# Performance work log

Hardware: AMD Instinct MI355X
Metric: run time of the kernel (lower is better)

The kernel has to match this reference:

```python
import jax, jax.numpy as jnp
import numpy as np

NUM_HEADS = 8


def setup_inputs() -> dict:
    key = jax.random.key(0)
    k1, k2, k3 = jax.random.split(key, 3)
    B, C, H, W = 2, 256, 64, 64
    x = jax.random.normal(k1, (B, C, H, W), dtype=jnp.float32)
    # 1x1 conv kernels flattened to [out_ch, in_ch]
    w_qkv = jax.random.normal(k2, (3 * C, C), dtype=jnp.float32) * (1.0 / np.sqrt(C))
    w_proj = jax.random.normal(k3, (C, C), dtype=jnp.float32) * (1.0 / np.sqrt(C))
    return {"x": x, "w_qkv": w_qkv, "w_proj": w_proj}


def reference(x, w_qkv, w_proj):
    B, C, H, W = x.shape
    h = NUM_HEADS
    hc = C // h  # head_channels
    scale = hc ** (-0.5)

    # 1x1 conv == per-pixel matmul over channels
    qkv = jnp.einsum('bchw,oc->bohw', x, w_qkv)  # [B, 3C, H, W]
    q, k, v = jnp.split(qkv, 3, axis=1)          # each [B, C, H, W]

    def to_heads(t):
        # 'b (h c) x y -> b h (x y) c'
        return t.reshape(B, h, hc, H * W).transpose(0, 1, 3, 2)

    q, k, v = to_heads(q), to_heads(k), to_heads(v)  # [B, h, N, hc]

    attn = jax.nn.softmax(jnp.einsum('bhnc,bhmc->bhnm', q, k) * scale, axis=-1)
    out = jnp.einsum('bhnm,bhmc->bhnc', attn, v)     # [B, h, N, hc]

    # 'b h (x y) c -> b (h c) x y'
    out = out.transpose(0, 1, 3, 2).reshape(B, C, H, W)
    return jnp.einsum('bchw,oc->bohw', out, w_proj)
```

## Files before the change

kernel.cpp:

```cpp
#include <hip/hip_runtime.h>
#include <hip/hip_bf16.h>


typedef short s8v __attribute__((ext_vector_type(8)));
typedef float f32x16 __attribute__((ext_vector_type(16)));
typedef float f32x2 __attribute__((ext_vector_type(2)));
typedef unsigned int u32;
typedef unsigned int u32x4 __attribute__((ext_vector_type(4)));

__device__ __forceinline__ u32 cvt_pk_bf16(float lo, float hi){
  u32 d;
  asm("v_cvt_pk_bf16_f32 %0, %1, %2" : "=v"(d) : "v"(lo), "v"(hi));
  return d;
}

__device__ __forceinline__ int frag_off(int row, int c){
  return ((c>>4)<<9) + (((c>>3)&1)<<8) + (row<<3) + (c&7);
}

__global__ __launch_bounds__(256) void k_transpose_cast(const float* __restrict__ x,
                                                        __hip_bfloat16* __restrict__ xt){
  __shared__ float tile[64][65];
  const int b = blockIdx.z;
  const int c0 = blockIdx.y * 64, p0 = blockIdx.x * 64;
  const int tx = threadIdx.x & 63, ty = threadIdx.x >> 6;
  const float* src = x + ((size_t)b*256 + c0)*4096 + p0;
#pragma unroll
  for(int i=0;i<16;i++){
    int r = i*4 + ty;
    tile[r][tx] = src[(size_t)r*4096 + tx];
  }
  __syncthreads();
  __hip_bfloat16* dstb = xt + (size_t)b*1048576;
#pragma unroll
  for(int it=0; it<2; ++it){
    int id = it*256 + threadIdx.x;
    int pl = id & 63, cc = id >> 6;
    int c = c0 + cc*8;
    u32x4 wv;
    wv.x = cvt_pk_bf16(tile[cc*8+0][pl], tile[cc*8+1][pl]);
    wv.y = cvt_pk_bf16(tile[cc*8+2][pl], tile[cc*8+3][pl]);
    wv.z = cvt_pk_bf16(tile[cc*8+4][pl], tile[cc*8+5][pl]);
    wv.w = cvt_pk_bf16(tile[cc*8+6][pl], tile[cc*8+7][pl]);
    int panel = (p0 + pl) >> 5;
    *(u32x4*)(dstb + (size_t)panel*8192 + frag_off(pl & 31, c)) = wv;
  }
}

__global__ __launch_bounds__(256) void k_cast_w(const float* __restrict__ wqkv,
                                                const float* __restrict__ wproj,
                                                __hip_bfloat16* __restrict__ wq,
                                                __hip_bfloat16* __restrict__ wp){
  int e = blockIdx.x*256 + threadIdx.x;
  const float* srcw; __hip_bfloat16* dstw;
  if(e < 24576){ srcw = wqkv; dstw = wq; }
  else { e -= 24576; srcw = wproj; dstw = wp; }
  int o = e >> 5, c0 = (e & 31)*8;
  const float* s = srcw + (size_t)o*256 + c0;
  u32x4 wv;
  wv.x = cvt_pk_bf16(s[0], s[1]);
  wv.y = cvt_pk_bf16(s[2], s[3]);
  wv.z = cvt_pk_bf16(s[4], s[5]);
  wv.w = cvt_pk_bf16(s[6], s[7]);
  *(u32x4*)(dstw + (size_t)(o>>5)*8192 + frag_off(o & 31, c0)) = wv;
}

__global__ __launch_bounds__(256) void k_qkv(const __hip_bfloat16* __restrict__ w,
                                             const __hip_bfloat16* __restrict__ xt,
                                             __hip_bfloat16* __restrict__ qb,
                                             __hip_bfloat16* __restrict__ kb,
                                             __hip_bfloat16* __restrict__ vt){
  const int wave = threadIdx.x >> 6, lane = threadIdx.x & 63;
  const int l31 = lane & 31, hi = lane >> 5;
  const int t = blockIdx.x*4 + wave;
  const int ntp = t & 127, mtp = t >> 7;
  const __hip_bfloat16* a0 = w  + (size_t)(2*mtp)*8192 + lane*8;
  const __hip_bfloat16* b0 = xt + (size_t)(2*ntp)*8192 + lane*8;
  f32x16 acc00, acc01, acc10, acc11;
#pragma unroll
  for(int i=0;i<16;i++){ acc00[i]=0.f; acc01[i]=0.f; acc10[i]=0.f; acc11[i]=0.f; }
#pragma unroll
  for(int kk=0;kk<16;kk++){
    s8v af0 = *(const s8v*)(a0 + kk*512);
    s8v af1 = *(const s8v*)(a0 + 8192 + kk*512);
    s8v bf0 = *(const s8v*)(b0 + kk*512);
    s8v bf1 = *(const s8v*)(b0 + 8192 + kk*512);
    acc00 = __builtin_amdgcn_mfma_f32_32x32x16_bf16(af0, bf0, acc00, 0,0,0);
    acc01 = __builtin_amdgcn_mfma_f32_32x32x16_bf16(af0, bf1, acc01, 0,0,0);
    acc10 = __builtin_amdgcn_mfma_f32_32x32x16_bf16(af1, bf0, acc10, 0,0,0);
    acc11 = __builtin_amdgcn_mfma_f32_32x32x16_bf16(af1, bf1, acc11, 0,0,0);
  }
  const int region = mtp >> 2;
  const float s = (region==0) ? (0.17677669529663687f * 1.4426950408889634f) : 1.0f;
#pragma unroll
  for(int mi=0; mi<2; ++mi){
#pragma unroll
    for(int ni=0; ni<2; ++ni){
      const f32x16& acc = (mi==0) ? (ni==0?acc00:acc01) : (ni==0?acc10:acc11);
      const int mt = 2*mtp + mi, nt = 2*ntp + ni;
      const int bb = nt >> 7, ktile = nt & 127, h = mt & 7;
      const size_t tbase = (size_t)(bb*8 + h)*131072 + (size_t)ktile*1024;
      if(region < 2){
        __hip_bfloat16* dst = (region==0 ? qb : kb) + tbase + l31*8 + 4*hi;
#pragma unroll
        for(int g=0; g<4; ++g){
          uint2 wv;
          wv.x = cvt_pk_bf16(acc[4*g+0]*s, acc[4*g+1]*s);
          wv.y = cvt_pk_bf16(acc[4*g+2]*s, acc[4*g+3]*s);
          *(uint2*)(dst + (g>>1)*512 + (g&1)*256) = wv;
        }
      } else {
        const int j = l31 >> 4, hv = (l31 >> 2) & 1, tt = ((l31>>3)&1)*4 + (l31&3);
        __hip_bfloat16* dst = vt + tbase + j*512 + hv*256 + tt;
#pragma unroll
        for(int r=0;r<16;++r){
          int c = (r&3) + 8*(r>>2) + 4*hi;
          dst[c*8] = __float2bfloat16(acc[r]);
        }
      }
    }
  }
}

__global__ __launch_bounds__(256, 4) void k_attn(const __hip_bfloat16* __restrict__ qb,
                                                 const __hip_bfloat16* __restrict__ kb,
                                                 const __hip_bfloat16* __restrict__ vt,
                                                 __hip_bfloat16* __restrict__ ost){
  __shared__ float part[4][64][33];
  __shared__ float lsl[4][64];
  const int wave = threadIdx.x >> 6, lane = threadIdx.x & 63;
  const int l31 = lane & 31, hi = lane >> 5;
  const int vid = (blockIdx.x & 7)*128 + (blockIdx.x >> 3);
  const int bh = vid >> 6, qc = vid & 63;

  const __hip_bfloat16* qt = qb + (size_t)bh*131072 + (size_t)(qc*2)*1024 + (size_t)lane*8;
  const s8v qfA0 = *(const s8v*)qt;
  const s8v qfA1 = *(const s8v*)(qt + 512);
  const s8v qfB0 = *(const s8v*)(qt + 1024);
  const s8v qfB1 = *(const s8v*)(qt + 1536);

  const __hip_bfloat16* kbase = kb + (size_t)bh*131072 + (size_t)lane*8;
  const __hip_bfloat16* vbase = vt + (size_t)bh*131072 + (size_t)lane*8;

  f32x16 zf;
#pragma unroll
  for(int i=0;i<16;i++) zf[i]=0.f;
  f32x16 oaccA, oaccB;
#pragma unroll
  for(int i=0;i<16;i++){ oaccA[i]=0.f; oaccB[i]=0.f; }
  f32x2 sA0={0.f,0.f}, sA1={0.f,0.f}, sB0={0.f,0.f}, sB1={0.f,0.f};

  const int kt0 = wave*32;
#pragma unroll 2
  for(int i=0;i<32;++i){
    const int kt = kt0 + i;
    const __hip_bfloat16* kp = kbase + (size_t)kt*1024;
    s8v kf0 = *(const s8v*)kp, kf1 = *(const s8v*)(kp + 512);
    f32x16 saA = __builtin_amdgcn_mfma_f32_32x32x16_bf16(kf0, qfA0, zf, 0,0,0);
    saA = __builtin_amdgcn_mfma_f32_32x32x16_bf16(kf1, qfA1, saA, 0,0,0);
    f32x16 saB = __builtin_amdgcn_mfma_f32_32x32x16_bf16(kf0, qfB0, zf, 0,0,0);
    saB = __builtin_amdgcn_mfma_f32_32x32x16_bf16(kf1, qfB1, saB, 0,0,0);

    float pvA[16], pvB[16];
#pragma unroll
    for(int r=0;r<16;++r) pvA[r] = __builtin_amdgcn_exp2f(saA[r]);
#pragma unroll
    for(int r=0;r<16;++r) pvB[r] = __builtin_amdgcn_exp2f(saB[r]);
    sA0 += (f32x2){pvA[0],pvA[1]};   sA1 += (f32x2){pvA[2],pvA[3]};
    sA0 += (f32x2){pvA[4],pvA[5]};   sA1 += (f32x2){pvA[6],pvA[7]};
    sA0 += (f32x2){pvA[8],pvA[9]};   sA1 += (f32x2){pvA[10],pvA[11]};
    sA0 += (f32x2){pvA[12],pvA[13]}; sA1 += (f32x2){pvA[14],pvA[15]};
    sB0 += (f32x2){pvB[0],pvB[1]};   sB1 += (f32x2){pvB[2],pvB[3]};
    sB0 += (f32x2){pvB[4],pvB[5]};   sB1 += (f32x2){pvB[6],pvB[7]};
    sB0 += (f32x2){pvB[8],pvB[9]};   sB1 += (f32x2){pvB[10],pvB[11]};
    sB0 += (f32x2){pvB[12],pvB[13]}; sB1 += (f32x2){pvB[14],pvB[15]};

    u32x4 wA0, wA1, wB0, wB1;
    wA0.x = cvt_pk_bf16(pvA[0],  pvA[1]);   wA0.y = cvt_pk_bf16(pvA[2],  pvA[3]);
    wA0.z = cvt_pk_bf16(pvA[4],  pvA[5]);   wA0.w = cvt_pk_bf16(pvA[6],  pvA[7]);
    wA1.x = cvt_pk_bf16(pvA[8],  pvA[9]);   wA1.y = cvt_pk_bf16(pvA[10], pvA[11]);
    wA1.z = cvt_pk_bf16(pvA[12], pvA[13]);  wA1.w = cvt_pk_bf16(pvA[14], pvA[15]);
    wB0.x = cvt_pk_bf16(pvB[0],  pvB[1]);   wB0.y = cvt_pk_bf16(pvB[2],  pvB[3]);
    wB0.z = cvt_pk_bf16(pvB[4],  pvB[5]);   wB0.w = cvt_pk_bf16(pvB[6],  pvB[7]);
    wB1.x = cvt_pk_bf16(pvB[8],  pvB[9]);   wB1.y = cvt_pk_bf16(pvB[10], pvB[11]);
    wB1.z = cvt_pk_bf16(pvB[12], pvB[13]);  wB1.w = cvt_pk_bf16(pvB[14], pvB[15]);

    const __hip_bfloat16* vp = vbase + (size_t)kt*1024;
    s8v vf0 = *(const s8v*)vp, vf1 = *(const s8v*)(vp + 512);
    oaccA = __builtin_amdgcn_mfma_f32_32x32x16_bf16(vf0, __builtin_bit_cast(s8v, wA0), oaccA, 0,0,0);
    oaccA = __builtin_amdgcn_mfma_f32_32x32x16_bf16(vf1, __builtin_bit_cast(s8v, wA1), oaccA, 0,0,0);
    oaccB = __builtin_amdgcn_mfma_f32_32x32x16_bf16(vf0, __builtin_bit_cast(s8v, wB0), oaccB, 0,0,0);
    oaccB = __builtin_amdgcn_mfma_f32_32x32x16_bf16(vf1, __builtin_bit_cast(s8v, wB1), oaccB, 0,0,0);
  }

  float lsumA = (sA0.x + sA0.y) + (sA1.x + sA1.y);
  float lsumB = (sB0.x + sB0.y) + (sB1.x + sB1.y);
  lsumA += __shfl_xor(lsumA, 32, 64);
  lsumB += __shfl_xor(lsumB, 32, 64);
  lsl[wave][l31] = lsumA;
  lsl[wave][32 + l31] = lsumB;
#pragma unroll
  for(int r=0;r<16;++r){
    int c = (r&3) + 8*(r>>2) + 4*hi;
    part[wave][l31][c] = oaccA[r];
    part[wave][32 + l31][c] = oaccB[r];
  }
  __syncthreads();

  const int b = bh >> 3, h = bh & 7;
  __hip_bfloat16* obase = ost + (size_t)(b*128 + qc*2)*8192;
#pragma unroll
  for(int it=0; it<8; ++it){
    int e = it*256 + threadIdx.x;
    int q = e >> 5, c = e & 31;
    float o = (part[0][q][c] + part[1][q][c]) + (part[2][q][c] + part[3][q][c]);
    float L = (lsl[0][q] + lsl[1][q]) + (lsl[2][q] + lsl[3][q]);
    obase[(size_t)(q>>5)*8192 + (h*2 + (c>>4))*512 + ((c>>3)&1)*256 + (q&31)*8 + (c&7)]
        = __float2bfloat16(o / L);
  }
}

__global__ __launch_bounds__(256) void k_proj(const __hip_bfloat16* __restrict__ w,
                                              const __hip_bfloat16* __restrict__ ost,
                                              float* __restrict__ out){
  const int wave = threadIdx.x >> 6, lane = threadIdx.x & 63;
  const int l31 = lane & 31, hi = lane >> 5;
  const int t = blockIdx.x*4 + wave;
  const int nt = t & 255, mt = t >> 8;
  const __hip_bfloat16* arow = w   + (size_t)mt*8192 + lane*8;
  const __hip_bfloat16* brow = ost + (size_t)nt*8192 + lane*8;
  f32x16 acc;
#pragma unroll
  for(int i=0;i<16;i++) acc[i]=0.f;
#pragma unroll
  for(int kk=0;kk<16;kk++){
    s8v a = *(const s8v*)(arow + kk*512);
    s8v b = *(const s8v*)(brow + kk*512);
    acc = __builtin_amdgcn_mfma_f32_32x32x16_bf16(a, b, acc, 0,0,0);
  }
  const int pg = nt*32 + l31;
  const int bb = pg >> 12, p = pg & 4095;
  float* dst = out + (size_t)bb*1048576 + p;
#pragma unroll
  for(int r=0;r<16;++r){
    int o = mt*32 + (r&3) + 8*(r>>2) + 4*hi;
    dst[(size_t)o*4096] = acc[r];
  }
}

extern "C" void kernel_launch(void* const* d_in, const int* in_sizes, int n_in,
                              void* d_out, int out_size, void* d_ws, size_t ws_size,
                              hipStream_t stream){
  const float* x     = (const float*)d_in[0];
  const float* wqkv  = (const float*)d_in[1];
  const float* wproj = (const float*)d_in[2];
  float* out = (float*)d_out;

  const size_t SZ_XT = (size_t)8192*256*2;
  const size_t SZ_VT = (size_t)16*32*4096*2;
  const size_t SZ_WQ = (size_t)768*256*2;
  const size_t SZ_WP = (size_t)256*256*2;
  if(ws_size < SZ_XT + SZ_VT + SZ_WQ + SZ_WP) return;

  char* ws = (char*)d_ws;
  __hip_bfloat16* xt  = (__hip_bfloat16*)ws;
  __hip_bfloat16* vt  = (__hip_bfloat16*)(ws + SZ_XT);
  __hip_bfloat16* wqb = (__hip_bfloat16*)(ws + SZ_XT + SZ_VT);
  __hip_bfloat16* wpb = (__hip_bfloat16*)(ws + SZ_XT + SZ_VT + SZ_WQ);
  __hip_bfloat16* qb  = (__hip_bfloat16*)d_out;
  __hip_bfloat16* kb  = qb + (size_t)2*1024*1024;
  __hip_bfloat16* ost = xt;

  k_cast_w<<<128, 256, 0, stream>>>(wqkv, wproj, wqb, wpb);
  k_transpose_cast<<<dim3(64,4,2), 256, 0, stream>>>(x, xt);
  k_qkv<<<384, 256, 0, stream>>>(wqb, xt, qb, kb, vt);
  k_attn<<<1024, 256, 0, stream>>>(qb, kb, vt, ost);
  k_proj<<<512, 256, 0, stream>>>(wpb, ost, out);
}
```

Measured before the change: 76.39 us.

## Fuse weight cast into prep kernel and software-pipeline global loads in GEMMs and attention

```diff
diff --git a/kernel.cpp b/kernel.cpp
--- a/kernel.cpp
+++ b/kernel.cpp
@@ -18,8 +18,12 @@
   return ((c>>4)<<9) + (((c>>3)&1)<<8) + (row<<3) + (c&7);
 }
 
-__global__ __launch_bounds__(256) void k_transpose_cast(const float* __restrict__ x,
-                                                        __hip_bfloat16* __restrict__ xt){
+__global__ __launch_bounds__(256) void k_prep(const float* __restrict__ x,
+                                              const float* __restrict__ wqkv,
+                                              const float* __restrict__ wproj,
+                                              __hip_bfloat16* __restrict__ xt,
+                                              __hip_bfloat16* __restrict__ wq,
+                                              __hip_bfloat16* __restrict__ wp){
   __shared__ float tile[64][65];
   const int b = blockIdx.z;
   const int c0 = blockIdx.y * 64, p0 = blockIdx.x * 64;
@@ -29,6 +33,21 @@
   for(int i=0;i<16;i++){
     int r = i*4 + ty;
     tile[r][tx] = src[(size_t)r*4096 + tx];
+  }
+  if(threadIdx.x < 64){
+    int flat = (blockIdx.z*4 + blockIdx.y)*64 + blockIdx.x;
+    int e = flat*64 + threadIdx.x;
+    const float* srcw; __hip_bfloat16* dstw;
+    if(e < 24576){ srcw = wqkv; dstw = wq; }
+    else { e -= 24576; srcw = wproj; dstw = wp; }
+    int o = e >> 5, cw = (e & 31)*8;
+    const float* s = srcw + (size_t)o*256 + cw;
+    u32x4 wv;
+    wv.x = cvt_pk_bf16(s[0], s[1]);
+    wv.y = cvt_pk_bf16(s[2], s[3]);
+    wv.z = cvt_pk_bf16(s[4], s[5]);
+    wv.w = cvt_pk_bf16(s[6], s[7]);
+    *(u32x4*)(dstw + (size_t)(o>>5)*8192 + frag_off(o & 31, cw)) = wv;
   }
   __syncthreads();
   __hip_bfloat16* dstb = xt + (size_t)b*1048576;
@@ -45,24 +64,6 @@
     int panel = (p0 + pl) >> 5;
     *(u32x4*)(dstb + (size_t)panel*8192 + frag_off(pl & 31, c)) = wv;
   }
-}
-
-__global__ __launch_bounds__(256) void k_cast_w(const float* __restrict__ wqkv,
-                                                const float* __restrict__ wproj,
-                                                __hip_bfloat16* __restrict__ wq,
-                                                __hip_bfloat16* __restrict__ wp){
-  int e = blockIdx.x*256 + threadIdx.x;
-  const float* srcw; __hip_bfloat16* dstw;
-  if(e < 24576){ srcw = wqkv; dstw = wq; }
-  else { e -= 24576; srcw = wproj; dstw = wp; }
-  int o = e >> 5, c0 = (e & 31)*8;
-  const float* s = srcw + (size_t)o*256 + c0;
-  u32x4 wv;
-  wv.x = cvt_pk_bf16(s[0], s[1]);
-  wv.y = cvt_pk_bf16(s[2], s[3]);
-  wv.z = cvt_pk_bf16(s[4], s[5]);
-  wv.w = cvt_pk_bf16(s[6], s[7]);
-  *(u32x4*)(dstw + (size_t)(o>>5)*8192 + frag_off(o & 31, c0)) = wv;
 }
 
 __global__ __launch_bounds__(256) void k_qkv(const __hip_bfloat16* __restrict__ w,
@@ -79,17 +80,24 @@
   f32x16 acc00, acc01, acc10, acc11;
 #pragma unroll
   for(int i=0;i<16;i++){ acc00[i]=0.f; acc01[i]=0.f; acc10[i]=0.f; acc11[i]=0.f; }
-#pragma unroll
-  for(int kk=0;kk<16;kk++){
-    s8v af0 = *(const s8v*)(a0 + kk*512);
-    s8v af1 = *(const s8v*)(a0 + 8192 + kk*512);
-    s8v bf0 = *(const s8v*)(b0 + kk*512);
-    s8v bf1 = *(const s8v*)(b0 + 8192 + kk*512);
+  s8v af0 = *(const s8v*)a0,            af1 = *(const s8v*)(a0 + 8192);
+  s8v bf0 = *(const s8v*)b0,            bf1 = *(const s8v*)(b0 + 8192);
+  for(int kk=0;kk<15;kk++){
+    const __hip_bfloat16* an = a0 + (kk+1)*512;
+    const __hip_bfloat16* bn = b0 + (kk+1)*512;
+    s8v na0 = *(const s8v*)an, na1 = *(const s8v*)(an + 8192);
+    s8v nb0 = *(const s8v*)bn, nb1 = *(const s8v*)(bn + 8192);
     acc00 = __builtin_amdgcn_mfma_f32_32x32x16_bf16(af0, bf0, acc00, 0,0,0);
     acc01 = __builtin_amdgcn_mfma_f32_32x32x16_bf16(af0, bf1, acc01, 0,0,0);
     acc10 = __builtin_amdgcn_mfma_f32_32x32x16_bf16(af1, bf0, acc10, 0,0,0);
     acc11 = __builtin_amdgcn_mfma_f32_32x32x16_bf16(af1, bf1, acc11, 0,0,0);
-  }
+    af0 = na0; af1 = na1; bf0 = nb0; bf1 = nb1;
+  }
+  acc00 = __builtin_amdgcn_mfma_f32_32x32x16_bf16(af0, bf0, acc00, 0,0,0);
+  acc01 = __builtin_amdgcn_mfma_f32_32x32x16_bf16(af0, bf1, acc01, 0,0,0);
+  acc10 = __builtin_amdgcn_mfma_f32_32x32x16_bf16(af1, bf0, acc10, 0,0,0);
+  acc11 = __builtin_amdgcn_mfma_f32_32x32x16_bf16(af1, bf1, acc11, 0,0,0);
+
   const int region = mtp >> 2;
   const float s = (region==0) ? (0.17677669529663687f * 1.4426950408889634f) : 1.0f;
 #pragma unroll
@@ -139,8 +147,8 @@
   const s8v qfB0 = *(const s8v*)(qt + 1024);
   const s8v qfB1 = *(const s8v*)(qt + 1536);
 
-  const __hip_bfloat16* kbase = kb + (size_t)bh*131072 + (size_t)lane*8;
-  const __hip_bfloat16* vbase = vt + (size_t)bh*131072 + (size_t)lane*8;
+  const __hip_bfloat16* kp = kb + (size_t)bh*131072 + (size_t)(wave*32)*1024 + (size_t)lane*8;
+  const __hip_bfloat16* vp = vt + (size_t)bh*131072 + (size_t)(wave*32)*1024 + (size_t)lane*8;
 
   f32x16 zf;
 #pragma unroll
@@ -150,17 +158,13 @@
   for(int i=0;i<16;i++){ oaccA[i]=0.f; oaccB[i]=0.f; }
   f32x2 sA0={0.f,0.f}, sA1={0.f,0.f}, sB0={0.f,0.f}, sB1={0.f,0.f};
 
-  const int kt0 = wave*32;
-#pragma unroll 2
-  for(int i=0;i<32;++i){
-    const int kt = kt0 + i;
-    const __hip_bfloat16* kp = kbase + (size_t)kt*1024;
-    s8v kf0 = *(const s8v*)kp, kf1 = *(const s8v*)(kp + 512);
+  auto compute = [&](s8v kf0, s8v kf1, s8v vf0, s8v vf1){
+    __builtin_amdgcn_s_setprio(1);
     f32x16 saA = __builtin_amdgcn_mfma_f32_32x32x16_bf16(kf0, qfA0, zf, 0,0,0);
     saA = __builtin_amdgcn_mfma_f32_32x32x16_bf16(kf1, qfA1, saA, 0,0,0);
     f32x16 saB = __builtin_amdgcn_mfma_f32_32x32x16_bf16(kf0, qfB0, zf, 0,0,0);
     saB = __builtin_amdgcn_mfma_f32_32x32x16_bf16(kf1, qfB1, saB, 0,0,0);
-
+    __builtin_amdgcn_s_setprio(0);
     float pvA[16], pvB[16];
 #pragma unroll
     for(int r=0;r<16;++r) pvA[r] = __builtin_amdgcn_exp2f(saA[r]);
@@ -185,13 +189,25 @@
     wB1.x = cvt_pk_bf16(pvB[8],  pvB[9]);   wB1.y = cvt_pk_bf16(pvB[10], pvB[11]);
     wB1.z = cvt_pk_bf16(pvB[12], pvB[13]);  wB1.w = cvt_pk_bf16(pvB[14], pvB[15]);
 
-    const __hip_bfloat16* vp = vbase + (size_t)kt*1024;
-    s8v vf0 = *(const s8v*)vp, vf1 = *(const s8v*)(vp + 512);
+    __builtin_amdgcn_s_setprio(1);
     oaccA = __builtin_amdgcn_mfma_f32_32x32x16_bf16(vf0, __builtin_bit_cast(s8v, wA0), oaccA, 0,0,0);
     oaccA = __builtin_amdgcn_mfma_f32_32x32x16_bf16(vf1, __builtin_bit_cast(s8v, wA1), oaccA, 0,0,0);
     oaccB = __builtin_amdgcn_mfma_f32_32x32x16_bf16(vf0, __builtin_bit_cast(s8v, wB0), oaccB, 0,0,0);
     oaccB = __builtin_amdgcn_mfma_f32_32x32x16_bf16(vf1, __builtin_bit_cast(s8v, wB1), oaccB, 0,0,0);
-  }
+    __builtin_amdgcn_s_setprio(0);
+  };
+
+  s8v kf0 = *(const s8v*)kp, kf1 = *(const s8v*)(kp + 512);
+  s8v vf0 = *(const s8v*)vp, vf1 = *(const s8v*)(vp + 512);
+  for(int i=0;i<31;++i){
+    const __hip_bfloat16* nkp = kp + (i+1)*1024;
+    const __hip_bfloat16* nvp = vp + (i+1)*1024;
+    s8v nk0 = *(const s8v*)nkp, nk1 = *(const s8v*)(nkp + 512);
+    s8v nv0 = *(const s8v*)nvp, nv1 = *(const s8v*)(nvp + 512);
+    compute(kf0, kf1, vf0, vf1);
+    kf0 = nk0; kf1 = nk1; vf0 = nv0; vf1 = nv1;
+  }
+  compute(kf0, kf1, vf0, vf1);
 
   float lsumA = (sA0.x + sA0.y) + (sA1.x + sA1.y);
   float lsumB = (sB0.x + sB0.y) + (sB1.x + sB1.y);
@@ -232,12 +248,14 @@
   f32x16 acc;
 #pragma unroll
   for(int i=0;i<16;i++) acc[i]=0.f;
-#pragma unroll
-  for(int kk=0;kk<16;kk++){
-    s8v a = *(const s8v*)(arow + kk*512);
-    s8v b = *(const s8v*)(brow + kk*512);
+  s8v a = *(const s8v*)arow, b = *(const s8v*)brow;
+  for(int kk=0;kk<15;kk++){
+    s8v na = *(const s8v*)(arow + (kk+1)*512);
+    s8v nb = *(const s8v*)(brow + (kk+1)*512);
     acc = __builtin_amdgcn_mfma_f32_32x32x16_bf16(a, b, acc, 0,0,0);
-  }
+    a = na; b = nb;
+  }
+  acc = __builtin_amdgcn_mfma_f32_32x32x16_bf16(a, b, acc, 0,0,0);
   const int pg = nt*32 + l31;
   const int bb = pg >> 12, p = pg & 4095;
   float* dst = out + (size_t)bb*1048576 + p;
@@ -271,8 +289,7 @@
   __hip_bfloat16* kb  = qb + (size_t)2*1024*1024;
   __hip_bfloat16* ost = xt;
 
-  k_cast_w<<<128, 256, 0, stream>>>(wqkv, wproj, wqb, wpb);
-  k_transpose_cast<<<dim3(64,4,2), 256, 0, stream>>>(x, xt);
+  k_prep<<<dim3(64,4,2), 256, 0, stream>>>(x, wqkv, wproj, xt, wqb, wpb);
   k_qkv<<<384, 256, 0, stream>>>(wqb, xt, qb, kb, vt);
   k_attn<<<1024, 256, 0, stream>>>(qb, kb, vt, ost);
   k_proj<<<512, 256, 0, stream>>>(wpb, ost, out);
```

Measured after the change: 71.99 us. 1.06x faster.
